# Optimization experiments

Measured on AMD Instinct MI355X. Metric: run time of the kernel, lower is better.

## Reference

```python
import jax, jax.numpy as jnp
import numpy as np

N = 8192       # paired user/item batch
D_IN = 10000   # interaction-vector length
H = 1024       # hidden width
E = 128        # shared embedding dim


def setup_inputs() -> dict:
    key = jax.random.key(0)
    ks = jax.random.split(key, 10)
    g = 5.0 / 3.0  # tanh gain used by the torch init

    def xavier(k, shape):
        fan_in, fan_out = shape
        std = g * np.sqrt(2.0 / (fan_in + fan_out))
        return jax.random.normal(k, shape, dtype=jnp.float32) * std

    return {
        "user_data": jax.random.normal(ks[0], (N, D_IN), dtype=jnp.float32),
        "item_data": jax.random.normal(ks[1], (N, D_IN), dtype=jnp.float32),
        "Wu1": xavier(ks[2], (D_IN, H)),
        "bu1": jnp.full((H,), 0.01, dtype=jnp.float32),
        "Wu2": xavier(ks[3], (H, E)),
        "bu2": jnp.full((E,), 0.01, dtype=jnp.float32),
        "Wi1": xavier(ks[4], (D_IN, H)),
        "bi1": jnp.full((H,), 0.01, dtype=jnp.float32),
        "Wi2": xavier(ks[5], (H, E)),
        "bi2": jnp.full((E,), 0.01, dtype=jnp.float32),
    }


def reference(user_data, item_data, Wu1, bu1, Wu2, bu2, Wi1, bi1, Wi2, bi2):
    # Encoders (dropout is identity at inference). PolyLinear: Linear -> ReLU -> Linear.
    p = jax.nn.relu(user_data @ Wu1 + bu1) @ Wu2 + bu2   # [N, E]
    q = jax.nn.relu(item_data @ Wi1 + bi1) @ Wi2 + bi2   # [N, E]
    # (p @ q.T).diag() == row-wise dot product; identical math, O(N*E) not O(N^2*E).
    return jnp.einsum("ne,ne->n", p, q)
```

## Files before the change

kernel.cpp:

```cpp
#include <hip/hip_runtime.h>
#include <hip/hip_bf16.h>
#include <stdint.h>

#define KP   10112
#define DIN  10000
#define NB   8192
#define HID  1024
#define EMB  128
#define NKT  313
#define NI   79

typedef __attribute__((ext_vector_type(8))) __bf16 bf16x8;
typedef __attribute__((ext_vector_type(4))) float  f32x4;
typedef __attribute__((ext_vector_type(4))) unsigned short ushort4v;

typedef const __attribute__((address_space(1))) void* gas_cp;
typedef __attribute__((address_space(3))) void* las_p;

__device__ __forceinline__ unsigned short f2bf(float f) {
    union { float f; unsigned u; } c; c.f = f;
    unsigned u = c.u;
    u += 0x7FFFu + ((u >> 16) & 1u);
    return (unsigned short)(u >> 16);
}

__global__ void conv_pad(const float* __restrict__ src, unsigned short* __restrict__ dst) {
    const int c4  = blockIdx.x * blockDim.x + threadIdx.x;
    const int row = blockIdx.y;
    if (c4 >= KP / 4) return;
    ushort4v o;
    if (c4 < DIN / 4) {
        float4 a = *(const float4*)(src + (size_t)row * DIN + (size_t)c4 * 4);
        o[0] = f2bf(a.x); o[1] = f2bf(a.y); o[2] = f2bf(a.z); o[3] = f2bf(a.w);
    } else {
        o[0] = o[1] = o[2] = o[3] = 0;
    }
    *(ushort4v*)(dst + (size_t)row * KP + (size_t)c4 * 4) = o;
}

__global__ void conv_transpose(const float* __restrict__ src, unsigned short* __restrict__ dst,
                               int K, int N, int Kp) {
    __shared__ float tile[64][33];
    const int tx = threadIdx.x & 31, ty = threadIdx.x >> 5;
    const int k0 = blockIdx.x * 64, n0 = blockIdx.y * 32;
#pragma unroll
    for (int j = 0; j < 8; ++j) {
        int k = k0 + ty + j * 8;
        tile[ty + j * 8][tx] = (k < K) ? src[(size_t)k * N + n0 + tx] : 0.0f;
    }
    __syncthreads();
#pragma unroll
    for (int j = 0; j < 4; ++j) {
        int n = n0 + ty + j * 8;
        unsigned short lo = f2bf(tile[2 * tx][ty + j * 8]);
        unsigned short hi = f2bf(tile[2 * tx + 1][ty + j * 8]);
        unsigned int packed = (unsigned int)lo | ((unsigned int)hi << 16);
        *(unsigned int*)(dst + (size_t)n * Kp + k0 + 2 * tx) = packed;
    }
}

__global__ __launch_bounds__(512, 2)
void gemm1_8p(const unsigned short* __restrict__ Abf,
              const unsigned short* __restrict__ W1t,
              const float* __restrict__ b1u, const float* __restrict__ b1i,
              unsigned short* __restrict__ H1) {
    __shared__ __align__(16) unsigned short lds_[81920];

    const int t  = threadIdx.x;
    const int lane = t & 63, wv = t >> 6;
    const int wm = wv >> 2, wn = wv & 3;
    const int rA = lane & 15, kg = lane >> 4;

    const int side = blockIdx.x >> 2, bn = blockIdx.x & 3, bm = blockIdx.y;

    const unsigned short* AbfS = Abf + (size_t)side * NB * KP;
    const unsigned short* W1tS = W1t + (size_t)side * HID * KP;
    const float* bias = side ? b1i : b1u;
    unsigned short* Cout = H1 + (size_t)side * NB * HID;

    const int rowSA = bm * 256 + (t >> 3);
    const int rowSB = bn * 256 + (t >> 3);
    const int kcl   = (((t & 7) ^ ((t >> 3) & 7))) * 8;

    const int xk0 = ((0 * 4 + kg) ^ (rA & 7)) * 8;
    const int xk1 = ((1 * 4 + kg) ^ (rA & 7)) * 8;

    f32x4 acc[8][4] = {};
    bf16x8 a[4][2], b[4][2];

    auto stA = [&](int tile, int h, int buf) {
        const unsigned short* s = AbfS + (size_t)(rowSA + h * 128) * KP + tile * 64 + kcl;
        __builtin_amdgcn_global_load_lds((gas_cp)s, (las_p)(lds_ + buf * 16384 + h * 8192 + wv * 512), 16, 0, 0);
        __builtin_amdgcn_global_load_lds((gas_cp)(s + (size_t)64 * KP), (las_p)(lds_ + buf * 16384 + h * 8192 + 4096 + wv * 512), 16, 0, 0);
    };
    auto stB = [&](int tile, int h, int par) {
        const unsigned short* s = W1tS + (size_t)(rowSB + h * 128) * KP + tile * 64 + kcl;
        __builtin_amdgcn_global_load_lds((gas_cp)s, (las_p)(lds_ + 49152 + par * 16384 + h * 8192 + wv * 512), 16, 0, 0);
        __builtin_amdgcn_global_load_lds((gas_cp)(s + (size_t)64 * KP), (las_p)(lds_ + 49152 + par * 16384 + h * 8192 + 4096 + wv * 512), 16, 0, 0);
    };
    auto rdA = [&](int buf, int mq) {
        const int aB = buf * 16384 + wm * 8192 + rA * 64;
#pragma unroll
        for (int j = 0; j < 4; ++j) {
            a[j][0] = *(const bf16x8*)(lds_ + aB + (mq * 4 + j) * 1024 + xk0);
            a[j][1] = *(const bf16x8*)(lds_ + aB + (mq * 4 + j) * 1024 + xk1);
        }
    };
    auto rdB = [&](int par, int nq) {
        const int bB = 49152 + par * 16384 + (wn >> 1) * 8192 + (wn & 1) * 4096 + rA * 64;
#pragma unroll
        for (int j = 0; j < 2; ++j) {
            b[nq * 2 + j][0] = *(const bf16x8*)(lds_ + bB + (nq * 2 + j) * 1024 + xk0);
            b[nq * 2 + j][1] = *(const bf16x8*)(lds_ + bB + (nq * 2 + j) * 1024 + xk1);
        }
    };
    auto mm = [&](int mq, int nq) {
#pragma unroll
        for (int j = 0; j < 4; ++j)
#pragma unroll
            for (int jj = 0; jj < 2; ++jj)
#pragma unroll
                for (int ks = 0; ks < 2; ++ks)
                    acc[mq * 4 + j][nq * 2 + jj] = __builtin_amdgcn_mfma_f32_16x16x32_bf16(
                        a[j][ks], b[nq * 2 + jj][ks], acc[mq * 4 + j][nq * 2 + jj], 0, 0, 0);
    };

#define SYNCA() do { __builtin_amdgcn_s_barrier(); \
                     asm volatile("s_waitcnt lgkmcnt(0)" ::: "memory"); \
                     __builtin_amdgcn_s_setprio(1); } while (0)
#define SYNCB() do { __builtin_amdgcn_s_setprio(0); __builtin_amdgcn_s_barrier(); } while (0)

    stA(0, 0, 0); stA(0, 1, 0);
    stB(0, 0, 0); stB(0, 1, 0);
    stA(1, 0, 1); stA(1, 1, 1);
    asm volatile("s_waitcnt vmcnt(4)" ::: "memory");
    __builtin_amdgcn_s_barrier();

    int cA0 = 0, cA1 = 1, nA = 2;
    for (int i = 0; i < NI - 1; ++i) {
        const int t1 = 2 * i + 1, t2 = 2 * i + 2, t3 = 2 * i + 3;
        rdA(cA0, 0); rdB(0, 0); stB(t1, 0, 1);
        SYNCA(); mm(0, 0); SYNCB();
        rdB(0, 1); stB(t1, 1, 1);
        SYNCA(); mm(0, 1); SYNCB();
        rdA(cA0, 1); stA(t2, 0, nA);
        SYNCA(); mm(1, 0); SYNCB();
        stA(t2, 1, nA);
        asm volatile("s_waitcnt vmcnt(4)" ::: "memory");
        SYNCA(); mm(1, 1); SYNCB();
        rdA(cA1, 0); rdB(1, 0); stB(t2, 0, 0);
        SYNCA(); mm(0, 0); SYNCB();
        rdB(1, 1); stB(t2, 1, 0);
        SYNCA(); mm(0, 1); SYNCB();
        rdA(cA1, 1); stA(t3, 0, cA0);
        SYNCA(); mm(1, 0); SYNCB();
        stA(t3, 1, cA0);
        asm volatile("s_waitcnt vmcnt(4)" ::: "memory");
        SYNCA(); mm(1, 1); SYNCB();
        int tmp = cA1; cA1 = cA0; cA0 = nA; nA = tmp;
    }
    {
        const int tl = 2 * NI - 1;
        rdA(cA0, 0); rdB(0, 0); stB(tl, 0, 1);
        SYNCA(); mm(0, 0); SYNCB();
        rdB(0, 1); stB(tl, 1, 1);
        SYNCA(); mm(0, 1); SYNCB();
        rdA(cA0, 1);
        SYNCA(); mm(1, 0); SYNCB();
        asm volatile("s_waitcnt vmcnt(0)" ::: "memory");
        SYNCA(); mm(1, 1); SYNCB();
        rdA(cA1, 0); rdB(1, 0);
        SYNCA(); mm(0, 0); SYNCB();
        rdB(1, 1);
        SYNCA(); mm(0, 1); SYNCB();
        rdA(cA1, 1);
        SYNCA(); mm(1, 0); SYNCB();
        SYNCA(); mm(1, 1);
        __builtin_amdgcn_s_setprio(0);
    }
#undef SYNCA
#undef SYNCB

    const int rowbase = bm * 256 + wm * 128 + kg * 4;
    const int colbase = bn * 256 + wn * 64 + rA;
#pragma unroll
    for (int ni = 0; ni < 4; ++ni) {
        const int col = colbase + ni * 16;
        const float bv = bias[col];
#pragma unroll
        for (int mi = 0; mi < 8; ++mi) {
#pragma unroll
            for (int rr = 0; rr < 4; ++rr) {
                float v = fmaxf(acc[mi][ni][rr] + bv, 0.0f);
                Cout[(size_t)(rowbase + mi * 16 + rr) * HID + col] = f2bf(v);
            }
        }
    }
}

__global__ __launch_bounds__(256, 4)
void gemm1_fused(const float* __restrict__ Au, const float* __restrict__ Ai,
                 const unsigned short* __restrict__ W1t,
                 const float* __restrict__ b1u, const float* __restrict__ b1i,
                 unsigned short* __restrict__ H1) {
    __shared__ unsigned short As[2 * 4096];
    __shared__ unsigned short Bs[2 * 4096];

    const int t = threadIdx.x, lane = t & 63, wave = t >> 6;
    const int wr = wave >> 1, wc = wave & 1, rA = lane & 15, kg = lane >> 4;

    const int id   = (blockIdx.z * gridDim.y + blockIdx.y) * 8 + blockIdx.x;
    const int pos  = (id & 7) * 128 + (id >> 3);
    const int side = pos >> 9;
    const int rr   = pos & 511;
    const int bm   = rr >> 3, bn = rr & 7;

    const float* Ap = side ? Ai : Au;
    const unsigned short* Bt = W1t + (size_t)side * HID * KP;
    const float* bias = side ? b1i : b1u;
    unsigned short* Cout = H1 + (size_t)side * NB * HID;

    const int arow = t >> 1;
    const float* gA = Ap + (size_t)(bm * 128 + arow) * DIN + (t & 1) * 16;
    const int aswz = (arow >> 1) & 3;
    const int aw0 = arow * 32 + ((((t & 1) * 2)     ^ aswz)) * 8;
    const int aw1 = arow * 32 + ((((t & 1) * 2 + 1) ^ aswz)) * 8;

    const int srcc = (t & 3) ^ ((t >> 3) & 3);
    const unsigned short* gB = Bt + (size_t)(bn * 128 + (t >> 2)) * KP + (size_t)srcc * 8;
    const int wst = wave * 512;

    f32x4 acc[4][4] = {};
    const int swz  = (rA >> 1) & 3;
    const int aoff = (wr * 64 + rA) * 32 + (kg ^ swz) * 8;
    const int boff = (wc * 64 + rA) * 32 + (kg ^ swz) * 8;

    float4 ar0, ar1, ar2, ar3;

    auto loadA = [&](int kt2) {
        const float* p = gA + (size_t)kt2 * 32;
        if (kt2 == NKT - 1 && (t & 1)) {
            ar0 = make_float4(0, 0, 0, 0); ar1 = ar0; ar2 = ar0; ar3 = ar0;
        } else {
            ar0 = *(const float4*)(p);
            ar1 = *(const float4*)(p + 4);
            ar2 = *(const float4*)(p + 8);
            ar3 = *(const float4*)(p + 12);
        }
    };
    auto writeA = [&](int buf) {
        bf16x8 v0, v1;
        v0[0] = (__bf16)ar0.x; v0[1] = (__bf16)ar0.y; v0[2] = (__bf16)ar0.z; v0[3] = (__bf16)ar0.w;
        v0[4] = (__bf16)ar1.x; v0[5] = (__bf16)ar1.y; v0[6] = (__bf16)ar1.z; v0[7] = (__bf16)ar1.w;
        v1[0] = (__bf16)ar2.x; v1[1] = (__bf16)ar2.y; v1[2] = (__bf16)ar2.z; v1[3] = (__bf16)ar2.w;
        v1[4] = (__bf16)ar3.x; v1[5] = (__bf16)ar3.y; v1[6] = (__bf16)ar3.z; v1[7] = (__bf16)ar3.w;
        *(bf16x8*)(As + buf * 4096 + aw0) = v0;
        *(bf16x8*)(As + buf * 4096 + aw1) = v1;
    };
    auto stageB = [&](int kt2) {
        const int bo = (kt2 & 1) * 4096;
        const unsigned short* p = gB + (size_t)kt2 * 32;
        __builtin_amdgcn_global_load_lds((gas_cp)p,                     (las_p)(Bs + bo + wst),        16, 0, 0);
        __builtin_amdgcn_global_load_lds((gas_cp)(p + (size_t)64 * KP), (las_p)(Bs + bo + wst + 2048), 16, 0, 0);
    };
    auto compute = [&](int buf) {
        const int ao = buf * 4096 + aoff, bo = buf * 4096 + boff;
        bf16x8 b0 = *(const bf16x8*)(Bs + bo);
        bf16x8 b1 = *(const bf16x8*)(Bs + bo + 512);
        bf16x8 b2 = *(const bf16x8*)(Bs + bo + 1024);
        bf16x8 b3 = *(const bf16x8*)(Bs + bo + 1536);
#pragma unroll
        for (int m = 0; m < 4; ++m) {
            bf16x8 av = *(const bf16x8*)(As + ao + m * 512);
            acc[m][0] = __builtin_amdgcn_mfma_f32_16x16x32_bf16(av, b0, acc[m][0], 0, 0, 0);
            acc[m][1] = __builtin_amdgcn_mfma_f32_16x16x32_bf16(av, b1, acc[m][1], 0, 0, 0);
            acc[m][2] = __builtin_amdgcn_mfma_f32_16x16x32_bf16(av, b2, acc[m][2], 0, 0, 0);
            acc[m][3] = __builtin_amdgcn_mfma_f32_16x16x32_bf16(av, b3, acc[m][3], 0, 0, 0);
        }
    };

    loadA(0);
    __builtin_amdgcn_sched_barrier(0);
    stageB(0);
    __builtin_amdgcn_sched_barrier(0);
    writeA(0);
    loadA(1);
    asm volatile("s_waitcnt lgkmcnt(0)" ::: "memory");
    __builtin_amdgcn_s_barrier();

    for (int kt = 0; kt < NKT - 2; ++kt) {
        asm volatile("s_waitcnt vmcnt(4)" ::: "memory");
        __builtin_amdgcn_s_barrier();
        writeA((kt + 1) & 1);
        __builtin_amdgcn_sched_barrier(0);
        stageB(kt + 1);
        __builtin_amdgcn_sched_barrier(0);
        loadA(kt + 2);
        compute(kt & 1);
        asm volatile("s_waitcnt lgkmcnt(0)" ::: "memory");
        __builtin_amdgcn_s_barrier();
    }
    asm volatile("s_waitcnt vmcnt(4)" ::: "memory");
    __builtin_amdgcn_s_barrier();
    writeA((NKT - 1) & 1);
    __builtin_amdgcn_sched_barrier(0);
    stageB(NKT - 1);
    compute((NKT - 2) & 1);
    asm volatile("s_waitcnt lgkmcnt(0)" ::: "memory");
    __builtin_amdgcn_s_barrier();
    asm volatile("s_waitcnt vmcnt(0)" ::: "memory");
    __builtin_amdgcn_s_barrier();
    compute((NKT - 1) & 1);

    const int rowbase = bm * 128 + wr * 64 + kg * 4;
    const int colbase = bn * 128 + wc * 64 + rA;
#pragma unroll
    for (int n = 0; n < 4; ++n) {
        const int col = colbase + n * 16;
        const float bv = bias[col];
#pragma unroll
        for (int m = 0; m < 4; ++m) {
#pragma unroll
            for (int r = 0; r < 4; ++r) {
                float v = fmaxf(acc[m][n][r] + bv, 0.0f);
                Cout[(size_t)(rowbase + m * 16 + r) * HID + col] = f2bf(v);
            }
        }
    }
}

__global__ __launch_bounds__(256, 2)
void gemm2_fused(const unsigned short* __restrict__ H1,
                 const unsigned short* __restrict__ W2t,
                 const float* __restrict__ b2u, const float* __restrict__ b2i,
                 float* __restrict__ PQ) {
    __shared__ unsigned short As[3 * 4096];
    __shared__ unsigned short Bs[3 * 4096];

    const int t = threadIdx.x, lane = t & 63, wave = t >> 6;
    const int wr = wave >> 1, wc = wave & 1, rA = lane & 15, kg = lane >> 4;
    const int bm = blockIdx.y, side = blockIdx.z;
    const int nk = HID / 32;

    const unsigned short* A  = H1  + (size_t)side * NB * HID;
    const unsigned short* Bt = W2t + (size_t)side * EMB * HID;
    const float* bias = side ? b2i : b2u;
    float* Cout = PQ + (size_t)side * NB * EMB;

    const int srcc = (t & 3) ^ ((t >> 3) & 3);
    const unsigned short* ga = A  + (size_t)(bm * 128 + (t >> 2)) * HID + (size_t)srcc * 8;
    const unsigned short* gb = Bt + (size_t)(t >> 2) * HID + (size_t)srcc * 8;
    const size_t aP = (size_t)64 * HID;

    f32x4 acc[4][4] = {};
    const int swz  = (rA >> 1) & 3;
    const int aoff = (wr * 64 + rA) * 32 + (kg ^ swz) * 8;
    const int boff = (wc * 64 + rA) * 32 + (kg ^ swz) * 8;
    const int wst  = wave * 512;

    auto stage = [&](int buf) {
        const int bo = buf << 12;
        __builtin_amdgcn_global_load_lds((gas_cp)(ga),      (las_p)(As + bo + wst),        16, 0, 0);
        __builtin_amdgcn_global_load_lds((gas_cp)(ga + aP), (las_p)(As + bo + wst + 2048), 16, 0, 0);
        __builtin_amdgcn_global_load_lds((gas_cp)(gb),      (las_p)(Bs + bo + wst),        16, 0, 0);
        __builtin_amdgcn_global_load_lds((gas_cp)(gb + aP), (las_p)(Bs + bo + wst + 2048), 16, 0, 0);
        ga += 32; gb += 32;
    };
    auto compute = [&](int buf) {
        const int bo = buf << 12;
        bf16x8 af[4], bfr[4];
#pragma unroll
        for (int m = 0; m < 4; ++m) af[m]  = *(const bf16x8*)(As + bo + aoff + m * 512);
#pragma unroll
        for (int n = 0; n < 4; ++n) bfr[n] = *(const bf16x8*)(Bs + bo + boff + n * 512);
#pragma unroll
        for (int m = 0; m < 4; ++m)
#pragma unroll
            for (int n = 0; n < 4; ++n)
                acc[m][n] = __builtin_amdgcn_mfma_f32_16x16x32_bf16(af[m], bfr[n], acc[m][n], 0, 0, 0);
    };

    stage(0); stage(1);
    int cur = 0;
    for (int kt = 0; kt < nk - 2; ++kt) {
        int pfb = cur + 2; if (pfb >= 3) pfb -= 3;
        stage(pfb);
        asm volatile("s_waitcnt vmcnt(8)" ::: "memory");
        __builtin_amdgcn_s_barrier();
        compute(cur);
        __builtin_amdgcn_s_barrier();
        cur = (cur + 1 == 3) ? 0 : cur + 1;
    }
    asm volatile("s_waitcnt vmcnt(4)" ::: "memory");
    __builtin_amdgcn_s_barrier();
    compute(cur);
    cur = (cur + 1 == 3) ? 0 : cur + 1;
    asm volatile("s_waitcnt vmcnt(0)" ::: "memory");
    __builtin_amdgcn_s_barrier();
    compute(cur);

    const int rowbase = bm * 128 + wr * 64 + kg * 4;
    const int colbase = wc * 64 + rA;
#pragma unroll
    for (int n = 0; n < 4; ++n) {
        const int col = colbase + n * 16;
        const float bv = bias[col];
#pragma unroll
        for (int m = 0; m < 4; ++m) {
#pragma unroll
            for (int r = 0; r < 4; ++r) {
                Cout[(size_t)(rowbase + m * 16 + r) * EMB + col] = acc[m][n][r] + bv;
            }
        }
    }
}

__global__ void rowdot(const float* __restrict__ P, const float* __restrict__ Q,
                       float* __restrict__ out, int n) {
    int gid = blockIdx.x * blockDim.x + threadIdx.x;
    int w = gid >> 6, lane = gid & 63;
    if (w >= n) return;
    const float2 p = ((const float2*)(P + (size_t)w * EMB))[lane];
    const float2 q = ((const float2*)(Q + (size_t)w * EMB))[lane];
    float s = p.x * q.x + p.y * q.y;
#pragma unroll
    for (int off = 32; off; off >>= 1) s += __shfl_down(s, off);
    if (lane == 0) out[w] = s;
}

extern "C" void kernel_launch(void* const* d_in, const int* in_sizes, int n_in,
                              void* d_out, int out_size, void* d_ws, size_t ws_size,
                              hipStream_t stream) {
    const float* user = (const float*)d_in[0];
    const float* item = (const float*)d_in[1];
    const float* Wu1  = (const float*)d_in[2];
    const float* bu1  = (const float*)d_in[3];
    const float* Wu2  = (const float*)d_in[4];
    const float* bu2  = (const float*)d_in[5];
    const float* Wi1  = (const float*)d_in[6];
    const float* bi1  = (const float*)d_in[7];
    const float* Wi2  = (const float*)d_in[8];
    const float* bi2  = (const float*)d_in[9];
    float* out = (float*)d_out;

    char* ws = (char*)d_ws;
    size_t off = 0;
    auto alloc = [&](size_t bytes) {
        char* p = ws + off;
        off += (bytes + 255) & ~(size_t)255;
        return p;
    };

    unsigned short* W1t = (unsigned short*)alloc((size_t)2 * HID * KP * 2);
    unsigned short* W2t = (unsigned short*)alloc((size_t)2 * EMB * HID * 2);
    float* P  = (float*)alloc((size_t)NB * EMB * 4);
    float* Q  = (float*)alloc((size_t)NB * EMB * 4);
    unsigned short* H1 = (unsigned short*)alloc((size_t)2 * NB * HID * 2);

    const bool full = ws_size >= (off + (size_t)2 * NB * KP * 2 + (1u << 20));

    dim3 blk(256);
    conv_transpose<<<dim3(KP / 64, HID / 32), blk, 0, stream>>>(Wu1, W1t,                      DIN, HID, KP);
    conv_transpose<<<dim3(KP / 64, HID / 32), blk, 0, stream>>>(Wi1, W1t + (size_t)HID * KP,   DIN, HID, KP);
    conv_transpose<<<dim3(HID / 64, EMB / 32), blk, 0, stream>>>(Wu2, W2t,                     HID, EMB, HID);
    conv_transpose<<<dim3(HID / 64, EMB / 32), blk, 0, stream>>>(Wi2, W2t + (size_t)EMB * HID, HID, EMB, HID);

    if (full) {
        unsigned short* Abf = (unsigned short*)alloc((size_t)2 * NB * KP * 2);
        conv_pad<<<dim3((KP / 4 + 255) / 256, NB), blk, 0, stream>>>(user, Abf);
        conv_pad<<<dim3((KP / 4 + 255) / 256, NB), blk, 0, stream>>>(item, Abf + (size_t)NB * KP);
        gemm1_8p<<<dim3(8, 32), dim3(512), 0, stream>>>(Abf, W1t, bu1, bi1, H1);
    } else {
        gemm1_fused<<<dim3(8, 64, 2), blk, 0, stream>>>(user, item, W1t, bu1, bi1, H1);
    }
    gemm2_fused<<<dim3(1, 64, 2), blk, 0, stream>>>(H1, W2t, bu2, bi2, P);
    rowdot<<<(NB * 64) / 256, blk, 0, stream>>>(P, Q, out, NB);
}
```

Before: 510.4 us.

## Fuse fp32-to-bf16 activation conversion into the 256x256 first-layer GEMM

```diff
diff --git a/kernel.cpp b/kernel.cpp
--- a/kernel.cpp
+++ b/kernel.cpp
@@ -7,12 +7,10 @@
 #define NB   8192
 #define HID  1024
 #define EMB  128
-#define NKT  313
 #define NI   79
 
 typedef __attribute__((ext_vector_type(8))) __bf16 bf16x8;
 typedef __attribute__((ext_vector_type(4))) float  f32x4;
-typedef __attribute__((ext_vector_type(4))) unsigned short ushort4v;
 
 typedef const __attribute__((address_space(1))) void* gas_cp;
 typedef __attribute__((address_space(3))) void* las_p;
@@ -22,20 +20,6 @@
     unsigned u = c.u;
     u += 0x7FFFu + ((u >> 16) & 1u);
     return (unsigned short)(u >> 16);
-}
-
-__global__ void conv_pad(const float* __restrict__ src, unsigned short* __restrict__ dst) {
-    const int c4  = blockIdx.x * blockDim.x + threadIdx.x;
-    const int row = blockIdx.y;
-    if (c4 >= KP / 4) return;
-    ushort4v o;
-    if (c4 < DIN / 4) {
-        float4 a = *(const float4*)(src + (size_t)row * DIN + (size_t)c4 * 4);
-        o[0] = f2bf(a.x); o[1] = f2bf(a.y); o[2] = f2bf(a.z); o[3] = f2bf(a.w);
-    } else {
-        o[0] = o[1] = o[2] = o[3] = 0;
-    }
-    *(ushort4v*)(dst + (size_t)row * KP + (size_t)c4 * 4) = o;
 }
 
 __global__ void conv_transpose(const float* __restrict__ src, unsigned short* __restrict__ dst,
@@ -60,10 +44,10 @@
 }
 
 __global__ __launch_bounds__(512, 2)
-void gemm1_8p(const unsigned short* __restrict__ Abf,
-              const unsigned short* __restrict__ W1t,
-              const float* __restrict__ b1u, const float* __restrict__ b1i,
-              unsigned short* __restrict__ H1) {
+void gemm1_8pf(const float* __restrict__ Au, const float* __restrict__ Ai,
+               const unsigned short* __restrict__ W1t,
+               const float* __restrict__ b1u, const float* __restrict__ b1i,
+               unsigned short* __restrict__ H1) {
     __shared__ __align__(16) unsigned short lds_[81920];
 
     const int t  = threadIdx.x;
@@ -73,25 +57,47 @@
 
     const int side = blockIdx.x >> 2, bn = blockIdx.x & 3, bm = blockIdx.y;
 
-    const unsigned short* AbfS = Abf + (size_t)side * NB * KP;
+    const float* Asrc = side ? Ai : Au;
     const unsigned short* W1tS = W1t + (size_t)side * HID * KP;
     const float* bias = side ? b1i : b1u;
     unsigned short* Cout = H1 + (size_t)side * NB * HID;
 
-    const int rowSA = bm * 256 + (t >> 3);
+    const int arow = t >> 3;
+    const int akc  = t & 7;
+    const float* gAr = Asrc + (size_t)(bm * 256 + arow) * DIN + akc * 8;
+    const int adst = arow * 64 + ((akc ^ (arow & 7)) * 8);
+
     const int rowSB = bn * 256 + (t >> 3);
-    const int kcl   = (((t & 7) ^ ((t >> 3) & 7))) * 8;
+    const int kcl   = ((t & 7) ^ ((t >> 3) & 7)) * 8;
 
     const int xk0 = ((0 * 4 + kg) ^ (rA & 7)) * 8;
     const int xk1 = ((1 * 4 + kg) ^ (rA & 7)) * 8;
 
     f32x4 acc[8][4] = {};
     bf16x8 a[4][2], b[4][2];
-
-    auto stA = [&](int tile, int h, int buf) {
-        const unsigned short* s = AbfS + (size_t)(rowSA + h * 128) * KP + tile * 64 + kcl;
-        __builtin_amdgcn_global_load_lds((gas_cp)s, (las_p)(lds_ + buf * 16384 + h * 8192 + wv * 512), 16, 0, 0);
-        __builtin_amdgcn_global_load_lds((gas_cp)(s + (size_t)64 * KP), (las_p)(lds_ + buf * 16384 + h * 8192 + 4096 + wv * 512), 16, 0, 0);
+    float4 R0, R1, R2, R3;
+
+    auto ldA = [&](int tile, int h) {
+        const int k0 = tile * 64 + akc * 8;
+        const float* p = gAr + (size_t)(h * 128) * DIN + tile * 64;
+        if (k0 < DIN) {
+            R0 = *(const float4*)(p);
+            R1 = *(const float4*)(p + 4);
+            R2 = *(const float4*)(p + (size_t)64 * DIN);
+            R3 = *(const float4*)(p + (size_t)64 * DIN + 4);
+        } else {
+            R0 = make_float4(0, 0, 0, 0); R1 = R0; R2 = R0; R3 = R0;
+        }
+    };
+    auto wrA = [&](int buf, int h) {
+        bf16x8 v0, v1;
+        v0[0] = (__bf16)R0.x; v0[1] = (__bf16)R0.y; v0[2] = (__bf16)R0.z; v0[3] = (__bf16)R0.w;
+        v0[4] = (__bf16)R1.x; v0[5] = (__bf16)R1.y; v0[6] = (__bf16)R1.z; v0[7] = (__bf16)R1.w;
+        v1[0] = (__bf16)R2.x; v1[1] = (__bf16)R2.y; v1[2] = (__bf16)R2.z; v1[3] = (__bf16)R2.w;
+        v1[4] = (__bf16)R3.x; v1[5] = (__bf16)R3.y; v1[6] = (__bf16)R3.z; v1[7] = (__bf16)R3.w;
+        unsigned short* d = lds_ + buf * 16384 + h * 8192 + adst;
+        *(bf16x8*)(d)        = v0;
+        *(bf16x8*)(d + 4096) = v1;
     };
     auto stB = [&](int tile, int h, int par) {
         const unsigned short* s = W1tS + (size_t)(rowSB + h * 128) * KP + tile * 64 + kcl;
@@ -130,40 +136,41 @@
                      __builtin_amdgcn_s_setprio(1); } while (0)
 #define SYNCB() do { __builtin_amdgcn_s_setprio(0); __builtin_amdgcn_s_barrier(); } while (0)
 
-    stA(0, 0, 0); stA(0, 1, 0);
     stB(0, 0, 0); stB(0, 1, 0);
-    stA(1, 0, 1); stA(1, 1, 1);
-    asm volatile("s_waitcnt vmcnt(4)" ::: "memory");
+    ldA(0, 0); wrA(0, 0);
+    ldA(0, 1); wrA(0, 1);
+    ldA(1, 0); wrA(1, 0);
+    ldA(1, 1); wrA(1, 1);
+    asm volatile("s_waitcnt vmcnt(0) lgkmcnt(0)" ::: "memory");
     __builtin_amdgcn_s_barrier();
 
     int cA0 = 0, cA1 = 1, nA = 2;
     for (int i = 0; i < NI - 1; ++i) {
         const int t1 = 2 * i + 1, t2 = 2 * i + 2, t3 = 2 * i + 3;
-        rdA(cA0, 0); rdB(0, 0); stB(t1, 0, 1);
+        rdA(cA0, 0); rdB(0, 0); stB(t1, 0, 1); ldA(t2, 0);
         SYNCA(); mm(0, 0); SYNCB();
         rdB(0, 1); stB(t1, 1, 1);
         SYNCA(); mm(0, 1); SYNCB();
-        rdA(cA0, 1); stA(t2, 0, nA);
+        rdA(cA0, 1); wrA(nA, 0); ldA(t2, 1);
         SYNCA(); mm(1, 0); SYNCB();
-        stA(t2, 1, nA);
-        asm volatile("s_waitcnt vmcnt(4)" ::: "memory");
+        wrA(nA, 1);
+        asm volatile("s_waitcnt vmcnt(0)" ::: "memory");
         SYNCA(); mm(1, 1); SYNCB();
-        rdA(cA1, 0); rdB(1, 0); stB(t2, 0, 0);
+        rdA(cA1, 0); rdB(1, 0); stB(t2, 0, 0); ldA(t3, 0);
         SYNCA(); mm(0, 0); SYNCB();
         rdB(1, 1); stB(t2, 1, 0);
         SYNCA(); mm(0, 1); SYNCB();
-        rdA(cA1, 1); stA(t3, 0, cA0);
+        rdA(cA1, 1); wrA(cA0, 0); ldA(t3, 1);
         SYNCA(); mm(1, 0); SYNCB();
-        stA(t3, 1, cA0);
-        asm volatile("s_waitcnt vmcnt(4)" ::: "memory");
+        wrA(cA0, 1);
+        asm volatile("s_waitcnt vmcnt(0)" ::: "memory");
         SYNCA(); mm(1, 1); SYNCB();
         int tmp = cA1; cA1 = cA0; cA0 = nA; nA = tmp;
     }
     {
-        const int tl = 2 * NI - 1;
-        rdA(cA0, 0); rdB(0, 0); stB(tl, 0, 1);
+        rdA(cA0, 0); rdB(0, 0); stB(2 * NI - 1, 0, 1);
         SYNCA(); mm(0, 0); SYNCB();
-        rdB(0, 1); stB(tl, 1, 1);
+        rdB(0, 1); stB(2 * NI - 1, 1, 1);
         SYNCA(); mm(0, 1); SYNCB();
         rdA(cA0, 1);
         SYNCA(); mm(1, 0); SYNCB();
@@ -193,137 +200,6 @@
             for (int rr = 0; rr < 4; ++rr) {
                 float v = fmaxf(acc[mi][ni][rr] + bv, 0.0f);
                 Cout[(size_t)(rowbase + mi * 16 + rr) * HID + col] = f2bf(v);
-            }
-        }
-    }
-}
-
-__global__ __launch_bounds__(256, 4)
-void gemm1_fused(const float* __restrict__ Au, const float* __restrict__ Ai,
-                 const unsigned short* __restrict__ W1t,
-                 const float* __restrict__ b1u, const float* __restrict__ b1i,
-                 unsigned short* __restrict__ H1) {
-    __shared__ unsigned short As[2 * 4096];
-    __shared__ unsigned short Bs[2 * 4096];
-
-    const int t = threadIdx.x, lane = t & 63, wave = t >> 6;
-    const int wr = wave >> 1, wc = wave & 1, rA = lane & 15, kg = lane >> 4;
-
-    const int id   = (blockIdx.z * gridDim.y + blockIdx.y) * 8 + blockIdx.x;
-    const int pos  = (id & 7) * 128 + (id >> 3);
-    const int side = pos >> 9;
-    const int rr   = pos & 511;
-    const int bm   = rr >> 3, bn = rr & 7;
-
-    const float* Ap = side ? Ai : Au;
-    const unsigned short* Bt = W1t + (size_t)side * HID * KP;
-    const float* bias = side ? b1i : b1u;
-    unsigned short* Cout = H1 + (size_t)side * NB * HID;
-
-    const int arow = t >> 1;
-    const float* gA = Ap + (size_t)(bm * 128 + arow) * DIN + (t & 1) * 16;
-    const int aswz = (arow >> 1) & 3;
-    const int aw0 = arow * 32 + ((((t & 1) * 2)     ^ aswz)) * 8;
-    const int aw1 = arow * 32 + ((((t & 1) * 2 + 1) ^ aswz)) * 8;
-
-    const int srcc = (t & 3) ^ ((t >> 3) & 3);
-    const unsigned short* gB = Bt + (size_t)(bn * 128 + (t >> 2)) * KP + (size_t)srcc * 8;
-    const int wst = wave * 512;
-
-    f32x4 acc[4][4] = {};
-    const int swz  = (rA >> 1) & 3;
-    const int aoff = (wr * 64 + rA) * 32 + (kg ^ swz) * 8;
-    const int boff = (wc * 64 + rA) * 32 + (kg ^ swz) * 8;
-
-    float4 ar0, ar1, ar2, ar3;
-
-    auto loadA = [&](int kt2) {
-        const float* p = gA + (size_t)kt2 * 32;
-        if (kt2 == NKT - 1 && (t & 1)) {
-            ar0 = make_float4(0, 0, 0, 0); ar1 = ar0; ar2 = ar0; ar3 = ar0;
-        } else {
-            ar0 = *(const float4*)(p);
-            ar1 = *(const float4*)(p + 4);
-            ar2 = *(const float4*)(p + 8);
-            ar3 = *(const float4*)(p + 12);
-        }
-    };
-    auto writeA = [&](int buf) {
-        bf16x8 v0, v1;
-        v0[0] = (__bf16)ar0.x; v0[1] = (__bf16)ar0.y; v0[2] = (__bf16)ar0.z; v0[3] = (__bf16)ar0.w;
-        v0[4] = (__bf16)ar1.x; v0[5] = (__bf16)ar1.y; v0[6] = (__bf16)ar1.z; v0[7] = (__bf16)ar1.w;
-        v1[0] = (__bf16)ar2.x; v1[1] = (__bf16)ar2.y; v1[2] = (__bf16)ar2.z; v1[3] = (__bf16)ar2.w;
-        v1[4] = (__bf16)ar3.x; v1[5] = (__bf16)ar3.y; v1[6] = (__bf16)ar3.z; v1[7] = (__bf16)ar3.w;
-        *(bf16x8*)(As + buf * 4096 + aw0) = v0;
-        *(bf16x8*)(As + buf * 4096 + aw1) = v1;
-    };
-    auto stageB = [&](int kt2) {
-        const int bo = (kt2 & 1) * 4096;
-        const unsigned short* p = gB + (size_t)kt2 * 32;
-        __builtin_amdgcn_global_load_lds((gas_cp)p,                     (las_p)(Bs + bo + wst),        16, 0, 0);
-        __builtin_amdgcn_global_load_lds((gas_cp)(p + (size_t)64 * KP), (las_p)(Bs + bo + wst + 2048), 16, 0, 0);
-    };
-    auto compute = [&](int buf) {
-        const int ao = buf * 4096 + aoff, bo = buf * 4096 + boff;
-        bf16x8 b0 = *(const bf16x8*)(Bs + bo);
-        bf16x8 b1 = *(const bf16x8*)(Bs + bo + 512);
-        bf16x8 b2 = *(const bf16x8*)(Bs + bo + 1024);
-        bf16x8 b3 = *(const bf16x8*)(Bs + bo + 1536);
-#pragma unroll
-        for (int m = 0; m < 4; ++m) {
-            bf16x8 av = *(const bf16x8*)(As + ao + m * 512);
-            acc[m][0] = __builtin_amdgcn_mfma_f32_16x16x32_bf16(av, b0, acc[m][0], 0, 0, 0);
-            acc[m][1] = __builtin_amdgcn_mfma_f32_16x16x32_bf16(av, b1, acc[m][1], 0, 0, 0);
-            acc[m][2] = __builtin_amdgcn_mfma_f32_16x16x32_bf16(av, b2, acc[m][2], 0, 0, 0);
-            acc[m][3] = __builtin_amdgcn_mfma_f32_16x16x32_bf16(av, b3, acc[m][3], 0, 0, 0);
-        }
-    };
-
-    loadA(0);
-    __builtin_amdgcn_sched_barrier(0);
-    stageB(0);
-    __builtin_amdgcn_sched_barrier(0);
-    writeA(0);
-    loadA(1);
-    asm volatile("s_waitcnt lgkmcnt(0)" ::: "memory");
-    __builtin_amdgcn_s_barrier();
-
-    for (int kt = 0; kt < NKT - 2; ++kt) {
-        asm volatile("s_waitcnt vmcnt(4)" ::: "memory");
-        __builtin_amdgcn_s_barrier();
-        writeA((kt + 1) & 1);
-        __builtin_amdgcn_sched_barrier(0);
-        stageB(kt + 1);
-        __builtin_amdgcn_sched_barrier(0);
-        loadA(kt + 2);
-        compute(kt & 1);
-        asm volatile("s_waitcnt lgkmcnt(0)" ::: "memory");
-        __builtin_amdgcn_s_barrier();
-    }
-    asm volatile("s_waitcnt vmcnt(4)" ::: "memory");
-    __builtin_amdgcn_s_barrier();
-    writeA((NKT - 1) & 1);
-    __builtin_amdgcn_sched_barrier(0);
-    stageB(NKT - 1);
-    compute((NKT - 2) & 1);
-    asm volatile("s_waitcnt lgkmcnt(0)" ::: "memory");
-    __builtin_amdgcn_s_barrier();
-    asm volatile("s_waitcnt vmcnt(0)" ::: "memory");
-    __builtin_amdgcn_s_barrier();
-    compute((NKT - 1) & 1);
-
-    const int rowbase = bm * 128 + wr * 64 + kg * 4;
-    const int colbase = bn * 128 + wc * 64 + rA;
-#pragma unroll
-    for (int n = 0; n < 4; ++n) {
-        const int col = colbase + n * 16;
-        const float bv = bias[col];
-#pragma unroll
-        for (int m = 0; m < 4; ++m) {
-#pragma unroll
-            for (int r = 0; r < 4; ++r) {
-                float v = fmaxf(acc[m][n][r] + bv, 0.0f);
-                Cout[(size_t)(rowbase + m * 16 + r) * HID + col] = f2bf(v);
             }
         }
     }
@@ -457,22 +333,13 @@
     float* Q  = (float*)alloc((size_t)NB * EMB * 4);
     unsigned short* H1 = (unsigned short*)alloc((size_t)2 * NB * HID * 2);
 
-    const bool full = ws_size >= (off + (size_t)2 * NB * KP * 2 + (1u << 20));
-
     dim3 blk(256);
     conv_transpose<<<dim3(KP / 64, HID / 32), blk, 0, stream>>>(Wu1, W1t,                      DIN, HID, KP);
     conv_transpose<<<dim3(KP / 64, HID / 32), blk, 0, stream>>>(Wi1, W1t + (size_t)HID * KP,   DIN, HID, KP);
     conv_transpose<<<dim3(HID / 64, EMB / 32), blk, 0, stream>>>(Wu2, W2t,                     HID, EMB, HID);
     conv_transpose<<<dim3(HID / 64, EMB / 32), blk, 0, stream>>>(Wi2, W2t + (size_t)EMB * HID, HID, EMB, HID);
 
-    if (full) {
-        unsigned short* Abf = (unsigned short*)alloc((size_t)2 * NB * KP * 2);
-        conv_pad<<<dim3((KP / 4 + 255) / 256, NB), blk, 0, stream>>>(user, Abf);
-        conv_pad<<<dim3((KP / 4 + 255) / 256, NB), blk, 0, stream>>>(item, Abf + (size_t)NB * KP);
-        gemm1_8p<<<dim3(8, 32), dim3(512), 0, stream>>>(Abf, W1t, bu1, bi1, H1);
-    } else {
-        gemm1_fused<<<dim3(8, 64, 2), blk, 0, stream>>>(user, item, W1t, bu1, bi1, H1);
-    }
+    gemm1_8pf<<<dim3(8, 32), dim3(512), 0, stream>>>(user, item, W1t, bu1, bi1, H1);
     gemm2_fused<<<dim3(1, 64, 2), blk, 0, stream>>>(H1, W2t, bu2, bi2, P);
     rowdot<<<(NB * 64) / 256, blk, 0, stream>>>(P, Q, out, NB);
 }
```

New measurement: 728.9 us. +42.8%, slower.
